# Optimization experiments

Measured on AMD Instinct MI355X. Metric: run time of the kernel, lower is better.

## Reference

```python
import jax, jax.numpy as jnp
import numpy as np

IN_H, IN_W = 512, 512
OUT_H, OUT_W = 512, 512
K = 8
BATCH = 64


def setup_inputs() -> dict:
    key = jax.random.key(0)
    k1, k2, k3 = jax.random.split(key, 3)
    inp = jax.random.normal(k1, (BATCH, IN_H, IN_W), dtype=jnp.float32)
    connections = jax.random.randint(k2, (OUT_H * OUT_W, K), 0, IN_H * IN_W, dtype=jnp.int32)
    bound = 1.0 / np.sqrt(K)
    weights = jax.random.uniform(k3, (OUT_H * OUT_W, K), dtype=jnp.float32, minval=-bound, maxval=bound)
    return {"input": inp, "connections": connections, "weights": weights}


def reference(input, connections, weights):
    # input: (B, H_in, W_in); connections/weights: (O, K) with O = OUT_H*OUT_W
    b = input.shape[0]
    x_flat = input.reshape(b, -1)                       # (B, N_in)
    gathered = jnp.take(x_flat, connections, axis=1)    # (B, O, K)
    out = jnp.einsum('bok,ok->bo', gathered, weights)   # (B, O)
    return out.reshape(b, OUT_H, OUT_W)
```

## Files before the change

### kernel.cpp

```cpp
#include <hip/hip_runtime.h>


#define IN_N  (512*512)
#define OUT_N (512*512)
#define BATCH 64
#define KCONN 8
#define TIDX  128

__device__ inline unsigned short f2bf(float f) {
    unsigned u; __builtin_memcpy(&u, &f, 4);
    u = (u + 0x7fffu + ((u >> 16) & 1u)) >> 16;
    return (unsigned short)u;
}
__device__ inline float bflo(unsigned u) {
    unsigned v = u << 16; float f; __builtin_memcpy(&f, &v, 4); return f;
}
__device__ inline float bfhi(unsigned u) {
    unsigned v = u & 0xffff0000u; float f; __builtin_memcpy(&f, &v, 4); return f;
}

__global__ __launch_bounds__(256) void transpose_kernel(const float* __restrict__ in,
                                                        unsigned short* __restrict__ xt) {
    __shared__ float lds[BATCH][TIDX + 1];
    const int t    = threadIdx.x;
    const int idx0 = blockIdx.x * TIDX;

    const int lb = t >> 5;
    const int lc = (t & 31) << 2;
#pragma unroll
    for (int p = 0; p < 8; ++p) {
        const int b = p * 8 + lb;
        float4 v = *(const float4*)(in + (size_t)b * IN_N + idx0 + lc);
        lds[b][lc + 0] = v.x;
        lds[b][lc + 1] = v.y;
        lds[b][lc + 2] = v.z;
        lds[b][lc + 3] = v.w;
    }
    __syncthreads();

    const int si = t >> 3;
    const int sb = (t & 7) << 3;
#pragma unroll
    for (int p = 0; p < 4; ++p) {
        const int i = p * 32 + si;
        union { unsigned short s[8]; uint4 v; } pk;
#pragma unroll
        for (int e = 0; e < 8; ++e) pk.s[e] = f2bf(lds[sb + e][i]);
        *(uint4*)(xt + (size_t)(idx0 + i) * BATCH + sb) = pk.v;
    }
}

__global__ __launch_bounds__(256, 4) void gather_kernel(const unsigned short* __restrict__ xt,
                                                        const int* __restrict__ conn,
                                                        const float* __restrict__ w,
                                                        float* __restrict__ out) {
    const int t  = threadIdx.x;
    const int o0 = blockIdx.x * 32;
    const int g  = o0 * KCONN + t;
    const int k  = t & 7;
    const int o  = o0 + (t >> 3);

    const int   ci = conn[g];
    const float wv = w[g];

    const uint4* row = (const uint4*)(xt + (size_t)ci * BATCH);
    uint4 r[8];
#pragma unroll
    for (int q = 0; q < 8; ++q) r[q] = row[q];

    float cur[64];
#pragma unroll
    for (int q = 0; q < 8; ++q) {
        const unsigned wq[4] = {r[q].x, r[q].y, r[q].z, r[q].w};
#pragma unroll
        for (int e = 0; e < 4; ++e) {
            cur[q * 8 + e * 2 + 0] = bflo(wq[e]) * wv;
            cur[q * 8 + e * 2 + 1] = bfhi(wq[e]) * wv;
        }
    }

    int bsel = 0;

    {
        const bool up = (k & 1) != 0;
        float nxt[32];
#pragma unroll
        for (int j = 0; j < 32; ++j) {
            float send = up ? cur[j] : cur[j + 32];
            float keep = up ? cur[j + 32] : cur[j];
            nxt[j] = keep + __shfl_xor(send, 1, 64);
        }
#pragma unroll
        for (int j = 0; j < 32; ++j) cur[j] = nxt[j];
        if (up) bsel += 32;
    }
    {
        const bool up = (k & 2) != 0;
        float nxt[16];
#pragma unroll
        for (int j = 0; j < 16; ++j) {
            float send = up ? cur[j] : cur[j + 16];
            float keep = up ? cur[j + 16] : cur[j];
            nxt[j] = keep + __shfl_xor(send, 2, 64);
        }
#pragma unroll
        for (int j = 0; j < 16; ++j) cur[j] = nxt[j];
        if (up) bsel += 16;
    }
    {
        const bool up = (k & 4) != 0;
        float nxt[8];
#pragma unroll
        for (int j = 0; j < 8; ++j) {
            float send = up ? cur[j] : cur[j + 8];
            float keep = up ? cur[j + 8] : cur[j];
            nxt[j] = keep + __shfl_xor(send, 4, 64);
        }
#pragma unroll
        for (int j = 0; j < 8; ++j) cur[j] = nxt[j];
        if (up) bsel += 8;
    }

#pragma unroll
    for (int j = 0; j < 8; ++j) {
        out[(size_t)(bsel + j) * OUT_N + o] = cur[j];
    }
}

__global__ __launch_bounds__(256) void direct_kernel(const float* __restrict__ in,
                                                     const int* __restrict__ conn,
                                                     const float* __restrict__ w,
                                                     float* __restrict__ out) {
    const int o = blockIdx.x * 256 + threadIdx.x;

    const int4   c0 = ((const int4*)conn)[(size_t)o * 2 + 0];
    const int4   c1 = ((const int4*)conn)[(size_t)o * 2 + 1];
    const float4 w0 = ((const float4*)w)[(size_t)o * 2 + 0];
    const float4 w1 = ((const float4*)w)[(size_t)o * 2 + 1];

    const int   cidx[KCONN] = {c0.x, c0.y, c0.z, c0.w, c1.x, c1.y, c1.z, c1.w};
    const float wk[KCONN]   = {w0.x, w0.y, w0.z, w0.w, w1.x, w1.y, w1.z, w1.w};

    for (int b = 0; b < BATCH; ++b) {
        const float* xb = in + (size_t)b * IN_N;
        float acc = 0.0f;
#pragma unroll
        for (int k = 0; k < KCONN; ++k) acc += xb[cidx[k]] * wk[k];
        out[(size_t)b * OUT_N + o] = acc;
    }
}

extern "C" void kernel_launch(void* const* d_in, const int* in_sizes, int n_in,
                              void* d_out, int out_size, void* d_ws, size_t ws_size,
                              hipStream_t stream) {
    const float* inp  = (const float*)d_in[0];
    const int*   conn = (const int*)d_in[1];
    const float* w    = (const float*)d_in[2];
    float*       out  = (float*)d_out;

    const size_t xt_bytes = (size_t)IN_N * BATCH * sizeof(unsigned short);

    if (ws_size >= xt_bytes) {
        unsigned short* xt = (unsigned short*)d_ws;
        transpose_kernel<<<IN_N / TIDX, 256, 0, stream>>>(inp, xt);
        gather_kernel<<<OUT_N / 32, 256, 0, stream>>>(xt, conn, w, out);
    } else {
        direct_kernel<<<OUT_N / 256, 256, 0, stream>>>(inp, conn, w, out);
    }
}
```

Baseline: 190.7 us.

## Split gather work by batch chunk per thread and pack bf16 before transpose

The gather kernel now has each thread own one output and an 8-wide batch slice, looping over all 8 connections with a 16-byte load each. This replaces the per-connection full-row load followed by a three-stage butterfly shuffle reduction, cutting register pressure and shuffle traffic. The transpose converts to bf16 before writing to LDS, which halves LDS size and LDS traffic. Occupancy hints rise to 8 waves. Each output's connection indices are now read by 8 threads, which relies on cache hits, and gather row reads become 16-byte pieces spread across lanes rather than contiguous full rows.

```diff
diff --git a/kernel.cpp b/kernel.cpp
--- a/kernel.cpp
+++ b/kernel.cpp
@@ -19,9 +19,9 @@
     unsigned v = u & 0xffff0000u; float f; __builtin_memcpy(&f, &v, 4); return f;
 }
 
-__global__ __launch_bounds__(256) void transpose_kernel(const float* __restrict__ in,
-                                                        unsigned short* __restrict__ xt) {
-    __shared__ float lds[BATCH][TIDX + 1];
+__global__ __launch_bounds__(256, 8) void transpose_kernel(const float* __restrict__ in,
+                                                           unsigned short* __restrict__ xt) {
+    __shared__ unsigned lds_u[BATCH][TIDX / 2 + 1];
     const int t    = threadIdx.x;
     const int idx0 = blockIdx.x * TIDX;
 
@@ -31,99 +31,68 @@
     for (int p = 0; p < 8; ++p) {
         const int b = p * 8 + lb;
         float4 v = *(const float4*)(in + (size_t)b * IN_N + idx0 + lc);
-        lds[b][lc + 0] = v.x;
-        lds[b][lc + 1] = v.y;
-        lds[b][lc + 2] = v.z;
-        lds[b][lc + 3] = v.w;
+        const unsigned u0 = (unsigned)f2bf(v.x) | ((unsigned)f2bf(v.y) << 16);
+        const unsigned u1 = (unsigned)f2bf(v.z) | ((unsigned)f2bf(v.w) << 16);
+        lds_u[b][(lc >> 1) + 0] = u0;
+        lds_u[b][(lc >> 1) + 1] = u1;
     }
     __syncthreads();
 
     const int si = t >> 3;
     const int sb = (t & 7) << 3;
 #pragma unroll
-    for (int p = 0; p < 4; ++p) {
-        const int i = p * 32 + si;
-        union { unsigned short s[8]; uint4 v; } pk;
+    for (int p = 0; p < 2; ++p) {
+        const int col = p * 32 + si;
+        unsigned lo[4], hi[4];
 #pragma unroll
-        for (int e = 0; e < 8; ++e) pk.s[e] = f2bf(lds[sb + e][i]);
-        *(uint4*)(xt + (size_t)(idx0 + i) * BATCH + sb) = pk.v;
+        for (int j = 0; j < 4; ++j) {
+            const unsigned a  = lds_u[sb + 2 * j + 0][col];
+            const unsigned b2 = lds_u[sb + 2 * j + 1][col];
+            lo[j] = (a & 0xffffu) | (b2 << 16);
+            hi[j] = (a >> 16) | (b2 & 0xffff0000u);
+        }
+        union { unsigned u[4]; uint4 v; } pk;
+        pk.u[0] = lo[0]; pk.u[1] = lo[1]; pk.u[2] = lo[2]; pk.u[3] = lo[3];
+        *(uint4*)(xt + (size_t)(idx0 + 2 * col + 0) * BATCH + sb) = pk.v;
+        pk.u[0] = hi[0]; pk.u[1] = hi[1]; pk.u[2] = hi[2]; pk.u[3] = hi[3];
+        *(uint4*)(xt + (size_t)(idx0 + 2 * col + 1) * BATCH + sb) = pk.v;
     }
 }
 
-__global__ __launch_bounds__(256, 4) void gather_kernel(const unsigned short* __restrict__ xt,
+__global__ __launch_bounds__(256, 8) void gather_kernel(const unsigned short* __restrict__ xt,
                                                         const int* __restrict__ conn,
                                                         const float* __restrict__ w,
                                                         float* __restrict__ out) {
     const int t  = threadIdx.x;
     const int o0 = blockIdx.x * 32;
-    const int g  = o0 * KCONN + t;
-    const int k  = t & 7;
-    const int o  = o0 + (t >> 3);
+    const int ol = t >> 3;
+    const int ch = t & 7;
+    const int o  = o0 + ol;
 
-    const int   ci = conn[g];
-    const float wv = w[g];
+    const int4   c0 = ((const int4*)conn)[(size_t)o * 2 + 0];
+    const int4   c1 = ((const int4*)conn)[(size_t)o * 2 + 1];
+    const float4 w0 = ((const float4*)w)[(size_t)o * 2 + 0];
+    const float4 w1 = ((const float4*)w)[(size_t)o * 2 + 1];
+    const int   cidx[KCONN] = {c0.x, c0.y, c0.z, c0.w, c1.x, c1.y, c1.z, c1.w};
+    const float wk[KCONN]   = {w0.x, w0.y, w0.z, w0.w, w1.x, w1.y, w1.z, w1.w};
 
-    const uint4* row = (const uint4*)(xt + (size_t)ci * BATCH);
-    uint4 r[8];
+    float acc[8] = {0.f, 0.f, 0.f, 0.f, 0.f, 0.f, 0.f, 0.f};
+
 #pragma unroll
-    for (int q = 0; q < 8; ++q) r[q] = row[q];
-
-    float cur[64];
-#pragma unroll
-    for (int q = 0; q < 8; ++q) {
-        const unsigned wq[4] = {r[q].x, r[q].y, r[q].z, r[q].w};
+    for (int k = 0; k < KCONN; ++k) {
+        const uint4 r = *(const uint4*)(xt + (size_t)cidx[k] * BATCH + ch * 8);
+        const unsigned q[4] = {r.x, r.y, r.z, r.w};
+        const float wv = wk[k];
 #pragma unroll
         for (int e = 0; e < 4; ++e) {
-            cur[q * 8 + e * 2 + 0] = bflo(wq[e]) * wv;
-            cur[q * 8 + e * 2 + 1] = bfhi(wq[e]) * wv;
+            acc[2 * e + 0] += bflo(q[e]) * wv;
+            acc[2 * e + 1] += bfhi(q[e]) * wv;
         }
-    }
-
-    int bsel = 0;
-
-    {
-        const bool up = (k & 1) != 0;
-        float nxt[32];
-#pragma unroll
-        for (int j = 0; j < 32; ++j) {
-            float send = up ? cur[j] : cur[j + 32];
-            float keep = up ? cur[j + 32] : cur[j];
-            nxt[j] = keep + __shfl_xor(send, 1, 64);
-        }
-#pragma unroll
-        for (int j = 0; j < 32; ++j) cur[j] = nxt[j];
-        if (up) bsel += 32;
-    }
-    {
-        const bool up = (k & 2) != 0;
-        float nxt[16];
-#pragma unroll
-        for (int j = 0; j < 16; ++j) {
-            float send = up ? cur[j] : cur[j + 16];
-            float keep = up ? cur[j + 16] : cur[j];
-            nxt[j] = keep + __shfl_xor(send, 2, 64);
-        }
-#pragma unroll
-        for (int j = 0; j < 16; ++j) cur[j] = nxt[j];
-        if (up) bsel += 16;
-    }
-    {
-        const bool up = (k & 4) != 0;
-        float nxt[8];
-#pragma unroll
-        for (int j = 0; j < 8; ++j) {
-            float send = up ? cur[j] : cur[j + 8];
-            float keep = up ? cur[j + 8] : cur[j];
-            nxt[j] = keep + __shfl_xor(send, 4, 64);
-        }
-#pragma unroll
-        for (int j = 0; j < 8; ++j) cur[j] = nxt[j];
-        if (up) bsel += 8;
     }
 
 #pragma unroll
     for (int j = 0; j < 8; ++j) {
-        out[(size_t)(bsel + j) * OUT_N + o] = cur[j];
+        out[(size_t)(ch * 8 + j) * OUT_N + o] = acc[j];
     }
 }
 
```

After: 178.7 us. 6.3% less time.
